# Kernel optimization log

Measured on AMD Instinct MI355X. Metric: run time of the kernel, lower is better.

## Reference

```python
import jax, jax.numpy as jnp
import numpy as np

B, LQ, LK, D, H, DK, DV = 8, 1024, 1024, 512, 8, 64, 64
EPS = 1e-14          # K.epsilon()**2 with default K.epsilon()=1e-7
MASK_VALUE = -1e30   # default mask_value in call()


def setup_inputs() -> dict:
    key = jax.random.key(0)
    ks = jax.random.split(key, 7)
    query = jax.random.normal(ks[0], (B, LQ, D), jnp.float32)
    key_t = jax.random.normal(ks[1], (B, LK, D), jnp.float32)
    value = jax.random.normal(ks[2], (B, LK, D), jnp.float32)
    mask = jax.random.randint(ks[3], (B, LK), 0, 2).astype(jnp.float32)
    glorot = np.sqrt(2.0 / (D + DK)).astype(np.float32)
    Wq = jax.random.normal(ks[4], (H, D, DK), jnp.float32) * glorot
    Wk = jax.random.normal(ks[5], (H, D, DK), jnp.float32) * glorot
    Wv = jax.random.normal(ks[6], (H, D, DV), jnp.float32) * glorot
    gamma = jnp.ones((1,), jnp.float32)
    beta = jnp.zeros((1,), jnp.float32)
    return {"query": query, "key": key_t, "value": value, "mask": mask,
            "Wq": Wq, "Wk": Wk, "Wv": Wv, "gamma": gamma, "beta": beta}


def reference(query, key, value, mask, Wq, Wk, Wv, gamma, beta):
    # Per-head projections (the original's Python loop over heads, vectorized).
    q = jnp.einsum('bqd,hde->bhqe', query, Wq)   # [B,H,LQ,DK]
    k = jnp.einsum('bkd,hde->bhke', key, Wk)     # [B,H,LK,DK]
    v = jnp.einsum('bkd,hde->bhke', value, Wv)   # [B,H,LK,DV]
    # NOTE: no 1/sqrt(dk) scaling, faithful to the source.
    A = jnp.einsum('bhqe,bhke->bhqk', q, k)      # [B,H,LQ,LK]
    m = mask[:, None, None, :]                    # [B,1,1,LK] broadcast over heads & queries
    A = m * A + (1.0 - m) * MASK_VALUE
    A = jax.nn.softmax(A, axis=-1)
    o = jnp.einsum('bhqk,bhke->bhqe', A, v)      # [B,H,LQ,DV]
    conc = o.transpose(0, 2, 1, 3).reshape(B, LQ, H * DV)  # concat heads
    # Scalar-affine layernorm over the concatenated feature dim.
    mean = jnp.mean(conc, axis=-1, keepdims=True)
    var = jnp.mean(jnp.square(conc - mean), axis=-1, keepdims=True)
    x = (conc - mean) / jnp.sqrt(var + EPS)
    return x * gamma[0] + beta[0]
```

## Files before the change

kernel.cpp:

```cpp
#include <hip/hip_runtime.h>
#include <math.h>

#define NB 8
#define NLQ 1024
#define NLK 1024
#define ND 512
#define NH 8
#define MASKV -1e30f
#define LOG2E 1.44269504088896f
#define SHIFT2 32.0f

typedef unsigned short ushort_t;
typedef __attribute__((ext_vector_type(8))) _Float16 f16x8;
typedef __attribute__((ext_vector_type(8))) short bf16x8;
typedef __attribute__((ext_vector_type(16))) float f32x16;

__device__ __forceinline__ ushort_t f2h_bits(float f) {
    union { _Float16 h; ushort_t u; } v; v.h = (_Float16)f;
    return v.u;
}
__device__ __forceinline__ ushort_t f2bf(float f) {
    union { float f; unsigned u; } v; v.f = f;
    unsigned r = v.u + 0x7fffu + ((v.u >> 16) & 1u);
    return (ushort_t)(r >> 16);
}
__device__ __forceinline__ void gload16(const ushort_t* g, ushort_t* l) {
    __builtin_amdgcn_global_load_lds(
        (const __attribute__((address_space(1))) void*)g,
        (__attribute__((address_space(3))) void*)l, 16, 0, 0);
}
__device__ __forceinline__ unsigned pack_bf16_trunc(float p0, float p1) {
    return __builtin_amdgcn_perm(__float_as_uint(p1), __float_as_uint(p0),
                                 0x07060302u);
}

__global__ __launch_bounds__(256) void wsplit_kernel(
    const float* __restrict__ Wq, const float* __restrict__ Wk, const float* __restrict__ Wv,
    ushort_t* __restrict__ oq, ushort_t* __restrict__ ok, ushort_t* __restrict__ ov) {
    __shared__ float T[64][65];
    const int d0 = blockIdx.x * 64;
    const int h  = blockIdx.y;
    const int t  = blockIdx.z;
    const float* W = (t == 0) ? Wq : (t == 1) ? Wk : Wv;
    ushort_t* oh = (t == 0) ? oq : (t == 1) ? ok : ov;
    const int tid = threadIdx.x;
#pragma unroll
    for (int i = 0; i < 4; i++) {
        int r = (tid >> 4) + i * 16;
        int c = (tid & 15) * 4;
        float4 v = *(const float4*)&W[((size_t)h * ND + d0 + r) * 64 + c];
        *(float4*)&T[r][c] = v;
    }
    __syncthreads();
    const int e = tid & 63;
    const int dg = tid >> 6;
    ushort_t hs[16];
#pragma unroll
    for (int dd = 0; dd < 16; dd++) hs[dd] = f2h_bits(T[dg * 16 + dd][e]);
    size_t base = ((size_t)h * 64 + e) * ND + d0 + dg * 16;
#pragma unroll
    for (int c = 0; c < 2; c++) {
        uint4 wh;
        wh.x = (unsigned)hs[8*c+0] | ((unsigned)hs[8*c+1] << 16);
        wh.y = (unsigned)hs[8*c+2] | ((unsigned)hs[8*c+3] << 16);
        wh.z = (unsigned)hs[8*c+4] | ((unsigned)hs[8*c+5] << 16);
        wh.w = (unsigned)hs[8*c+6] | ((unsigned)hs[8*c+7] << 16);
        *(uint4*)&oh[base + 8 * c] = wh;
    }
}

__global__ __launch_bounds__(256, 2) void proj_gemm_kernel(
    const float* __restrict__ Xq, const float* __restrict__ Xk,
    const float* __restrict__ Xv, const ushort_t* __restrict__ Wbase,
    ushort_t* __restrict__ Obase) {
    __shared__ ushort_t sA[2][8320];
    __shared__ ushort_t sB[2][8320];

    const int bid   = blockIdx.x;
    const int y     = bid / 192;
    const int mglob = bid % 192;
    const int t  = mglob >> 6;
    const int b  = (mglob >> 3) & 7;
    const int l0 = (mglob & 7) * 128;

    const int tid  = threadIdx.x;
    const int wave = tid >> 6;
    const int lane = tid & 63;
    const int l31  = lane & 31;
    const int hib  = lane >> 5;
    const int wr = wave >> 1, wc = wave & 1;

    const float* Xt = (t == 0) ? Xq : (t == 1) ? Xk : Xv;
    const float* gx = Xt + ((size_t)b * NLQ + l0) * ND;
    const ushort_t* gwt = Wbase + (size_t)t * ((size_t)NH * 64 * ND)
                        + (size_t)y * 128 * ND;
    ushort_t* out = Obase + (size_t)t * ((size_t)NB * NH * NLQ * 64);

    const int srow = lane >> 3;
    const int schk = (lane & 7) ^ srow;

    float4 ax[4][2];
    auto aload = [&](int d0) {
#pragma unroll
        for (int j = 0; j < 4; j++) {
            int row = (j * 4 + wave) * 8 + srow;
            const float* p = gx + (size_t)row * ND + d0 + schk * 8;
            ax[j][0] = *(const float4*)p;
            ax[j][1] = *(const float4*)(p + 4);
        }
    };
    auto awrite = [&](int buf) {
#pragma unroll
        for (int j = 0; j < 4; j++) {
            int u = j * 4 + wave;
            uint4 hv;
            hv.x = (unsigned)f2h_bits(ax[j][0].x) | ((unsigned)f2h_bits(ax[j][0].y) << 16);
            hv.y = (unsigned)f2h_bits(ax[j][0].z) | ((unsigned)f2h_bits(ax[j][0].w) << 16);
            hv.z = (unsigned)f2h_bits(ax[j][1].x) | ((unsigned)f2h_bits(ax[j][1].y) << 16);
            hv.w = (unsigned)f2h_bits(ax[j][1].z) | ((unsigned)f2h_bits(ax[j][1].w) << 16);
            *(uint4*)(sA[buf] + u * 520 + lane * 8) = hv;
        }
    };
    auto bstage = [&](int buf, int d0) {
#pragma unroll
        for (int j = 0; j < 4; j++) {
            int u = j * 4 + wave;
            int row = u * 8 + srow;
            gload16(gwt + (size_t)row * ND + d0 + schk * 8, sB[buf] + u * 520);
        }
    };

    f32x16 acc00, acc01, acc10, acc11;
#pragma unroll
    for (int i = 0; i < 16; i++) { acc00[i] = 0.f; acc01[i] = 0.f;
                                   acc10[i] = 0.f; acc11[i] = 0.f; }

    const int ga  = wr * 8 + (l31 >> 3);
    const int gb  = wc * 8 + (l31 >> 3);
    const int ro  = (l31 & 7) * 64;
    const int swz = l31 & 7;

    auto mfma_chunk = [&](int buf) {
#pragma unroll
        for (int c = 0; c < 4; c++) {
            const int pc = ((2 * c + hib) ^ swz) * 8;
            f16x8 a0 = *(const f16x8*)&sA[buf][ga * 520 + ro + pc];
            f16x8 a1 = *(const f16x8*)&sA[buf][(ga + 4) * 520 + ro + pc];
            f16x8 b0 = *(const f16x8*)&sB[buf][gb * 520 + ro + pc];
            f16x8 b1 = *(const f16x8*)&sB[buf][(gb + 4) * 520 + ro + pc];
            acc00 = __builtin_amdgcn_mfma_f32_32x32x16_f16(a0, b0, acc00, 0, 0, 0);
            acc01 = __builtin_amdgcn_mfma_f32_32x32x16_f16(a0, b1, acc01, 0, 0, 0);
            acc10 = __builtin_amdgcn_mfma_f32_32x32x16_f16(a1, b0, acc10, 0, 0, 0);
            acc11 = __builtin_amdgcn_mfma_f32_32x32x16_f16(a1, b1, acc11, 0, 0, 0);
        }
    };

    aload(0);
    bstage(0, 0);
    asm volatile("s_waitcnt vmcnt(4)" ::: "memory");
    __builtin_amdgcn_sched_barrier(0);
    awrite(0);
    aload(64);
    asm volatile("s_waitcnt vmcnt(8)" ::: "memory");
    asm volatile("s_waitcnt lgkmcnt(0)" ::: "memory");
    __builtin_amdgcn_sched_barrier(0);
    __builtin_amdgcn_s_barrier();

    int cur = 0;
#pragma unroll
    for (int kc = 0; kc < 8; kc++) {
        if (kc < 7) {
            bstage(cur ^ 1, (kc + 1) * 64);
            mfma_chunk(cur);
            asm volatile("s_waitcnt vmcnt(4)" ::: "memory");
            __builtin_amdgcn_sched_barrier(0);
            awrite(cur ^ 1);
            if (kc < 6) {
                aload((kc + 2) * 64);
                asm volatile("s_waitcnt vmcnt(8)" ::: "memory");
            } else {
                asm volatile("s_waitcnt vmcnt(0)" ::: "memory");
            }
            asm volatile("s_waitcnt lgkmcnt(0)" ::: "memory");
            __builtin_amdgcn_sched_barrier(0);
            __builtin_amdgcn_s_barrier();
        } else {
            mfma_chunk(cur);
        }
        cur ^= 1;
    }

    if (t < 2) {
        const float scale = (t == 0) ? LOG2E : 1.f;
#pragma unroll
        for (int mi = 0; mi < 2; mi++) {
#pragma unroll
            for (int ni = 0; ni < 2; ni++) {
                const f32x16& a = (mi == 0) ? (ni == 0 ? acc00 : acc01)
                                            : (ni == 0 ? acc10 : acc11);
                int nglob = y * 128 + wc * 64 + ni * 32 + l31;
                int hh = nglob >> 6, e = nglob & 63;
                size_t obase = (((size_t)b * NH + hh) * NLQ + l0) * 64 + e;
#pragma unroll
                for (int r = 0; r < 16; r++) {
                    int l = wr * 64 + mi * 32 + (r & 3) + 8 * (r >> 2) + 4 * hib;
                    out[obase + (size_t)l * 64] = f2h_bits(a[r] * scale);
                }
            }
        }
    } else {
        __syncthreads();
        ushort_t (*T)[130] = (ushort_t(*)[130])sA;
#pragma unroll
        for (int mi = 0; mi < 2; mi++) {
#pragma unroll
            for (int ni = 0; ni < 2; ni++) {
                const f32x16& a = (mi == 0) ? (ni == 0 ? acc00 : acc01)
                                            : (ni == 0 ? acc10 : acc11);
                int n_loc = wc * 64 + ni * 32 + l31;
#pragma unroll
                for (int r = 0; r < 16; r++) {
                    int l = wr * 64 + mi * 32 + (r & 3) + 8 * (r >> 2) + 4 * hib;
                    T[n_loc][l] = f2bf(a[r]);
                }
            }
        }
        __syncthreads();
        const int n_loc = tid >> 1;
        const int half  = tid & 1;
        const int hh = n_loc >> 6, e = n_loc & 63;
        size_t obase = (((size_t)b * NH + y * 2 + hh) * 64 + e) * NLK
                     + l0 + half * 64;
        const ushort_t* src = &T[n_loc][half * 64];
#pragma unroll
        for (int c2 = 0; c2 < 8; c2++)
            *(uint4*)&out[obase + c2 * 8] = *(const uint4*)&src[c2 * 8];
    }
}

__global__ __launch_bounds__(512, 2) void attn_kernel(
    const ushort_t* __restrict__ Qf, const ushort_t* __restrict__ Kf,
    const ushort_t* __restrict__ Vt, const float* __restrict__ maskp,
    float* __restrict__ Op) {
    __shared__ ushort_t sK[2][4160];
    __shared__ ushort_t sV[2][4160];
    __shared__ float sBias[1024];

    const int idx = blockIdx.x;
    const int bh_i = idx & 63;
    const int qc  = idx >> 6;
    const int b = bh_i >> 3, h = bh_i & 7;
    const size_t bh = (size_t)b * NH + h;

    const int tid  = threadIdx.x;
    const int wave = tid >> 6;
    const int lane = tid & 63;
    const int l31  = lane & 31;
    const int hib  = lane >> 5;
    const int q = qc * 256 + wave * 32 + l31;
    const int sw = l31 & 7;

    if (tid < 256) {
        const float* mrow = maskp + ((size_t)b << 10);
        float4 m0 = *(const float4*)&mrow[tid * 4];
        float4 bi;
        bi.x = (m0.x > 0.5f) ? -SHIFT2 : MASKV;
        bi.y = (m0.y > 0.5f) ? -SHIFT2 : MASKV;
        bi.z = (m0.z > 0.5f) ? -SHIFT2 : MASKV;
        bi.w = (m0.w > 0.5f) ? -SHIFT2 : MASKV;
        *(float4*)&sBias[tid * 4] = bi;
    }

    f16x8 qh[4];
    {
        const ushort_t* ph = Qf + (bh * NLQ + q) * 64 + hib * 8;
#pragma unroll
        for (int c = 0; c < 4; c++) qh[c] = *(const f16x8*)(ph + c * 16);
    }

    const int srow = lane >> 3;
    const int schk = (lane & 7) ^ srow;

    auto stage = [&](int buf, int k0) {
#pragma unroll
        for (int n = 0; n < 2; n++) {
            int u = wave + n * 8;
            if (u < 8) {
                int row = u * 8 + srow;
                int key = (row & ~12) | ((row & 4) << 1) | ((row & 8) >> 1);
                gload16(Kf + ((bh << 10) + k0 + key) * 64 + schk * 8,
                        sK[buf] + u * 520);
            } else {
                int u8 = u - 8;
                int row = u8 * 8 + srow;
                gload16(Vt + ((bh << 6) + row) * NLK + k0 + schk * 8,
                        sV[buf] + u8 * 520);
            }
        }
    };

    f32x16 O0, O1;
#pragma unroll
    for (int i = 0; i < 16; i++) { O0[i] = 0.f; O1[i] = 0.f; }
    float lrun = 0.f;

    const int rp0 = (l31 >> 3) * 520 + (l31 & 7) * 64;
    const int rp1 = rp0 + 4 * 520;

    stage(0, 0);
    __syncthreads();
    int cur = 0;

    for (int t = 0; t < 16; t++) {
        const int k0 = t << 6;
        if (t < 15) stage(cur ^ 1, k0 + 64);

        f32x16 S0, S1;
#pragma unroll
        for (int g = 0; g < 4; g++) {
            const int kb = k0 + 16 * (g >> 1) + 8 * hib + 4 * (g & 1);
            float4 b0 = *(const float4*)&sBias[kb];
            float4 b1 = *(const float4*)&sBias[kb + 32];
            S0[4 * g + 0] = b0.x; S0[4 * g + 1] = b0.y;
            S0[4 * g + 2] = b0.z; S0[4 * g + 3] = b0.w;
            S1[4 * g + 0] = b1.x; S1[4 * g + 1] = b1.y;
            S1[4 * g + 2] = b1.z; S1[4 * g + 3] = b1.w;
        }
#pragma unroll
        for (int c = 0; c < 4; c++) {
            const int pc = ((2 * c + hib) ^ sw) * 8;
            f16x8 a0 = *(const f16x8*)&sK[cur][rp0 + pc];
            f16x8 a1 = *(const f16x8*)&sK[cur][rp1 + pc];
            S0 = __builtin_amdgcn_mfma_f32_32x32x16_f16(a0, qh[c], S0, 0, 0, 0);
            S1 = __builtin_amdgcn_mfma_f32_32x32x16_f16(a1, qh[c], S1, 0, 0, 0);
        }

        unsigned pq[8][2];
#pragma unroll
        for (int g = 0; g < 8; g++) {
            float p0, p1, p2, p3;
            if (g < 4) {
                p0 = __builtin_amdgcn_exp2f(S0[4*g+0]);
                p1 = __builtin_amdgcn_exp2f(S0[4*g+1]);
                p2 = __builtin_amdgcn_exp2f(S0[4*g+2]);
                p3 = __builtin_amdgcn_exp2f(S0[4*g+3]);
            } else {
                p0 = __builtin_amdgcn_exp2f(S1[4*(g-4)+0]);
                p1 = __builtin_amdgcn_exp2f(S1[4*(g-4)+1]);
                p2 = __builtin_amdgcn_exp2f(S1[4*(g-4)+2]);
                p3 = __builtin_amdgcn_exp2f(S1[4*(g-4)+3]);
            }
            lrun += (p0 + p1) + (p2 + p3);
            pq[g][0] = pack_bf16_trunc(p0, p1);
            pq[g][1] = pack_bf16_trunc(p2, p3);
        }

#pragma unroll
        for (int c = 0; c < 4; c++) {
            union { unsigned u[4]; bf16x8 v; } pf;
            pf.u[0] = pq[2 * c][0];     pf.u[1] = pq[2 * c][1];
            pf.u[2] = pq[2 * c + 1][0]; pf.u[3] = pq[2 * c + 1][1];
            const int pc = ((2 * c + hib) ^ sw) * 8;
            bf16x8 v0 = *(const bf16x8*)&sV[cur][rp0 + pc];
            bf16x8 v1 = *(const bf16x8*)&sV[cur][rp1 + pc];
            O0 = __builtin_amdgcn_mfma_f32_32x32x16_bf16(v0, pf.v, O0, 0, 0, 0);
            O1 = __builtin_amdgcn_mfma_f32_32x32x16_bf16(v1, pf.v, O1, 0, 0, 0);
        }
        __syncthreads();
        cur ^= 1;
    }

    lrun += __shfl_xor(lrun, 32);
    const float linv = 1.f / lrun;
    float* obase = Op + ((size_t)(b * NLQ + q)) * (NH * 64) + h * 64;
#pragma unroll
    for (int me = 0; me < 2; me++) {
#pragma unroll
        for (int g = 0; g < 4; g++) {
            int e0 = me * 32 + 8 * g + 4 * hib;
            float4 o;
            if (me == 0) {
                o.x = O0[4 * g + 0] * linv; o.y = O0[4 * g + 1] * linv;
                o.z = O0[4 * g + 2] * linv; o.w = O0[4 * g + 3] * linv;
            } else {
                o.x = O1[4 * g + 0] * linv; o.y = O1[4 * g + 1] * linv;
                o.z = O1[4 * g + 2] * linv; o.w = O1[4 * g + 3] * linv;
            }
            *(float4*)&obase[e0] = o;
        }
    }
}

__global__ __launch_bounds__(256) void ln_kernel(const float* __restrict__ X,
                                                 const float* __restrict__ gamma,
                                                 const float* __restrict__ beta,
                                                 float* __restrict__ out) {
    const int row = blockIdx.x * 4 + (threadIdx.x >> 6);
    const int lane = threadIdx.x & 63;
    const float* x = &X[(size_t)row * 512];
    float4 v0 = *(const float4*)&x[lane * 8];
    float4 v1 = *(const float4*)&x[lane * 8 + 4];
    float sum = v0.x + v0.y + v0.z + v0.w + v1.x + v1.y + v1.z + v1.w;
    float sq = v0.x * v0.x + v0.y * v0.y + v0.z * v0.z + v0.w * v0.w
             + v1.x * v1.x + v1.y * v1.y + v1.z * v1.z + v1.w * v1.w;
#pragma unroll
    for (int off = 32; off > 0; off >>= 1) {
        sum += __shfl_down(sum, off);
        sq  += __shfl_down(sq, off);
    }
    sum = __shfl(sum, 0);
    sq  = __shfl(sq, 0);
    const float mean = sum * (1.f / 512.f);
    const float var = sq * (1.f / 512.f) - mean * mean;
    const float rstd = rsqrtf(var + 1e-14f);
    const float g = gamma[0], be = beta[0];
    float* o = &out[(size_t)row * 512];
    float4 r0, r1;
    r0.x = (v0.x - mean) * rstd * g + be;  r0.y = (v0.y - mean) * rstd * g + be;
    r0.z = (v0.z - mean) * rstd * g + be;  r0.w = (v0.w - mean) * rstd * g + be;
    r1.x = (v1.x - mean) * rstd * g + be;  r1.y = (v1.y - mean) * rstd * g + be;
    r1.z = (v1.z - mean) * rstd * g + be;  r1.w = (v1.w - mean) * rstd * g + be;
    *(float4*)&o[lane * 8] = r0;
    *(float4*)&o[lane * 8 + 4] = r1;
}

extern "C" void kernel_launch(void* const* d_in, const int* in_sizes, int n_in,
                              void* d_out, int out_size, void* d_ws, size_t ws_size,
                              hipStream_t stream) {
    const float* query = (const float*)d_in[0];
    const float* key_t = (const float*)d_in[1];
    const float* value = (const float*)d_in[2];
    const float* mask  = (const float*)d_in[3];
    const float* Wq    = (const float*)d_in[4];
    const float* Wk    = (const float*)d_in[5];
    const float* Wv    = (const float*)d_in[6];
    const float* gamma = (const float*)d_in[7];
    const float* beta  = (const float*)d_in[8];
    float* out = (float*)d_out;

    const size_t A = (size_t)NB * NLQ * ND;
    const size_t WS = (size_t)NH * 64 * ND;
    ushort_t* Qf = (ushort_t*)d_ws;
    ushort_t* Kf = Qf + A;
    ushort_t* Vt = Qf + 2 * A;
    ushort_t* Wt = Qf + 3 * A;

    wsplit_kernel<<<dim3(ND / 64, NH, 3), 256, 0, stream>>>(
        Wq, Wk, Wv, Wt, Wt + WS, Wt + 2 * WS);

    proj_gemm_kernel<<<768, 256, 0, stream>>>(
        query, key_t, value, Wt, Qf);

    attn_kernel<<<256, 512, 0, stream>>>(Qf, Kf, Vt, mask, out);

    ln_kernel<<<(NB * NLQ) / 4, 256, 0, stream>>>(out, gamma, beta, out);
}
```

Before: 162.9 us.

## Single-buffer A tile in registers to fit three projection blocks per CU

The projection GEMM now keeps one shared-memory A buffer and a double-buffered B. Each iteration first reads its A fragments into registers, then a barrier frees the A buffer so the next A tile can be written while the MFMAs run. This cuts shared memory per block from about 65 KB to about 49 KB, which allows launch bounds of 3 blocks per CU, so the 768-block grid can run in a single wave. In exchange, global A loads are prefetched only one step ahead instead of two, each step fully drains vmcnt, there is an extra barrier per step, and register pressure rises from holding the A fragments.

```diff
diff --git a/kernel.cpp b/kernel.cpp
--- a/kernel.cpp
+++ b/kernel.cpp
@@ -69,12 +69,14 @@
     }
 }
 
-__global__ __launch_bounds__(256, 2) void proj_gemm_kernel(
+__global__ __launch_bounds__(256, 3) void proj_gemm_kernel(
     const float* __restrict__ Xq, const float* __restrict__ Xk,
     const float* __restrict__ Xv, const ushort_t* __restrict__ Wbase,
     ushort_t* __restrict__ Obase) {
-    __shared__ ushort_t sA[2][8320];
-    __shared__ ushort_t sB[2][8320];
+    __shared__ ushort_t S[24960];
+    ushort_t* const sA  = S;
+    ushort_t* const sB0 = S + 8320;
+    ushort_t* const sB1 = S + 16640;
 
     const int bid   = blockIdx.x;
     const int y     = bid / 192;
@@ -109,7 +111,7 @@
             ax[j][1] = *(const float4*)(p + 4);
         }
     };
-    auto awrite = [&](int buf) {
+    auto awrite = [&]() {
 #pragma unroll
         for (int j = 0; j < 4; j++) {
             int u = j * 4 + wave;
@@ -118,15 +120,15 @@
             hv.y = (unsigned)f2h_bits(ax[j][0].z) | ((unsigned)f2h_bits(ax[j][0].w) << 16);
             hv.z = (unsigned)f2h_bits(ax[j][1].x) | ((unsigned)f2h_bits(ax[j][1].y) << 16);
             hv.w = (unsigned)f2h_bits(ax[j][1].z) | ((unsigned)f2h_bits(ax[j][1].w) << 16);
-            *(uint4*)(sA[buf] + u * 520 + lane * 8) = hv;
+            *(uint4*)(sA + u * 520 + lane * 8) = hv;
         }
     };
-    auto bstage = [&](int buf, int d0) {
+    auto bstage = [&](ushort_t* dst, int d0) {
 #pragma unroll
         for (int j = 0; j < 4; j++) {
             int u = j * 4 + wave;
             int row = u * 8 + srow;
-            gload16(gwt + (size_t)row * ND + d0 + schk * 8, sB[buf] + u * 520);
+            gload16(gwt + (size_t)row * ND + d0 + schk * 8, dst + u * 520);
         }
     };
 
@@ -140,54 +142,51 @@
     const int ro  = (l31 & 7) * 64;
     const int swz = l31 & 7;
 
-    auto mfma_chunk = [&](int buf) {
+    aload(0);
+    awrite();
+    bstage(sB0, 0);
+    asm volatile("s_waitcnt vmcnt(0) lgkmcnt(0)" ::: "memory");
+    __builtin_amdgcn_sched_barrier(0);
+    __builtin_amdgcn_s_barrier();
+    __builtin_amdgcn_sched_barrier(0);
+
+    ushort_t* sBc = sB0;
+    ushort_t* sBn = sB1;
+#pragma unroll
+    for (int kc = 0; kc < 8; kc++) {
+        if (kc < 7) aload((kc + 1) * 64);
+        f16x8 a0[4], a1[4];
 #pragma unroll
         for (int c = 0; c < 4; c++) {
             const int pc = ((2 * c + hib) ^ swz) * 8;
-            f16x8 a0 = *(const f16x8*)&sA[buf][ga * 520 + ro + pc];
-            f16x8 a1 = *(const f16x8*)&sA[buf][(ga + 4) * 520 + ro + pc];
-            f16x8 b0 = *(const f16x8*)&sB[buf][gb * 520 + ro + pc];
-            f16x8 b1 = *(const f16x8*)&sB[buf][(gb + 4) * 520 + ro + pc];
-            acc00 = __builtin_amdgcn_mfma_f32_32x32x16_f16(a0, b0, acc00, 0, 0, 0);
-            acc01 = __builtin_amdgcn_mfma_f32_32x32x16_f16(a0, b1, acc01, 0, 0, 0);
-            acc10 = __builtin_amdgcn_mfma_f32_32x32x16_f16(a1, b0, acc10, 0, 0, 0);
-            acc11 = __builtin_amdgcn_mfma_f32_32x32x16_f16(a1, b1, acc11, 0, 0, 0);
-        }
-    };
-
-    aload(0);
-    bstage(0, 0);
-    asm volatile("s_waitcnt vmcnt(4)" ::: "memory");
-    __builtin_amdgcn_sched_barrier(0);
-    awrite(0);
-    aload(64);
-    asm volatile("s_waitcnt vmcnt(8)" ::: "memory");
-    asm volatile("s_waitcnt lgkmcnt(0)" ::: "memory");
-    __builtin_amdgcn_sched_barrier(0);
-    __builtin_amdgcn_s_barrier();
-
-    int cur = 0;
-#pragma unroll
-    for (int kc = 0; kc < 8; kc++) {
+            a0[c] = *(const f16x8*)&sA[ga * 520 + ro + pc];
+            a1[c] = *(const f16x8*)&sA[(ga + 4) * 520 + ro + pc];
+        }
+        asm volatile("s_waitcnt lgkmcnt(0)" ::: "memory");
+        __builtin_amdgcn_sched_barrier(0);
+        __builtin_amdgcn_s_barrier();
+        __builtin_amdgcn_sched_barrier(0);
         if (kc < 7) {
-            bstage(cur ^ 1, (kc + 1) * 64);
-            mfma_chunk(cur);
-            asm volatile("s_waitcnt vmcnt(4)" ::: "memory");
-            __builtin_amdgcn_sched_barrier(0);
-            awrite(cur ^ 1);
-            if (kc < 6) {
-                aload((kc + 2) * 64);
-                asm volatile("s_waitcnt vmcnt(8)" ::: "memory");
-            } else {
-                asm volatile("s_waitcnt vmcnt(0)" ::: "memory");
-            }
-            asm volatile("s_waitcnt lgkmcnt(0)" ::: "memory");
+            bstage(sBn, (kc + 1) * 64);
+            awrite();
+        }
+#pragma unroll
+        for (int c = 0; c < 4; c++) {
+            const int pc = ((2 * c + hib) ^ swz) * 8;
+            f16x8 b0 = *(const f16x8*)&sBc[gb * 520 + ro + pc];
+            f16x8 b1 = *(const f16x8*)&sBc[(gb + 4) * 520 + ro + pc];
+            acc00 = __builtin_amdgcn_mfma_f32_32x32x16_f16(a0[c], b0, acc00, 0, 0, 0);
+            acc01 = __builtin_amdgcn_mfma_f32_32x32x16_f16(a0[c], b1, acc01, 0, 0, 0);
+            acc10 = __builtin_amdgcn_mfma_f32_32x32x16_f16(a1[c], b0, acc10, 0, 0, 0);
+            acc11 = __builtin_amdgcn_mfma_f32_32x32x16_f16(a1[c], b1, acc11, 0, 0, 0);
+        }
+        if (kc < 7) {
+            asm volatile("s_waitcnt vmcnt(0) lgkmcnt(0)" ::: "memory");
             __builtin_amdgcn_sched_barrier(0);
             __builtin_amdgcn_s_barrier();
-        } else {
-            mfma_chunk(cur);
-        }
-        cur ^= 1;
+            __builtin_amdgcn_sched_barrier(0);
+        }
+        ushort_t* tmp = sBc; sBc = sBn; sBn = tmp;
     }
 
     if (t < 2) {
@@ -210,7 +209,7 @@
         }
     } else {
         __syncthreads();
-        ushort_t (*T)[130] = (ushort_t(*)[130])sA;
+        ushort_t (*T)[130] = (ushort_t(*)[130])S;
 #pragma unroll
         for (int mi = 0; mi < 2; mi++) {
 #pragma unroll
```

After: 157.6 us. 3.3% less time.
